# Kernel tuning notes

Hardware: AMD Instinct MI355X
Metric: run time of the kernel (lower is better)

## Reference

```python
import jax, jax.numpy as jnp
import numpy as np

EPS = 1e-8          # EPSILON in source
THRESH = 0.5        # state.match_threshold
MIN_RADIUS = 0.05   # meaningful-observation threshold

B, T, H, D, N = 4, 4096, 2048, 256, 32768
Hq = H // 4


def setup_inputs() -> dict:
    key = jax.random.key(0)
    ks = jax.random.split(key, 10)
    s = 0.02
    return {
        "hidden": jax.random.normal(ks[0], (B, T, H), jnp.float32),
        "beliefs": jax.random.normal(ks[1], (N, D), jnp.float32),
        "active_mask": jax.random.bernoulli(ks[2], 0.5, (N,)),
        "W_obs": jax.random.normal(ks[3], (D, H), jnp.float32) * s,
        "W_g1": jax.random.normal(ks[4], (Hq, H), jnp.float32) * s,
        "b_g1": jnp.zeros((Hq,), jnp.float32),
        "W_g2": jax.random.normal(ks[5], (1, Hq), jnp.float32) * s,
        "b_g2": jnp.full((1,), -2.0, jnp.float32),  # nn.init.constant_(bias, -2.0)
        "W_p1": jax.random.normal(ks[6], (Hq, H), jnp.float32) * s,
        "b_p1": jnp.zeros((Hq,), jnp.float32),
        "W_p2": jax.random.normal(ks[7], (1, Hq), jnp.float32) * s,
        "b_p2": jnp.zeros((1,), jnp.float32),
    }


def reference(hidden, beliefs, active_mask, W_obs, W_g1, b_g1, W_g2, b_g2,
              W_p1, b_p1, W_p2, b_p2):
    # --- projections (torch Linear: y = x @ W.T + b) ---
    obs = jnp.einsum("bth,dh->btd", hidden, W_obs)                       # [B,T,D]
    gate = jax.nn.sigmoid(
        jnp.einsum("btq,oq->bto",
                   jax.nn.relu(jnp.einsum("bth,qh->btq", hidden, W_g1) + b_g1),
                   W_g2) + b_g2)                                          # [B,T,1]
    prec = jax.nn.softplus(
        jnp.einsum("btq,oq->bto",
                   jax.nn.relu(jnp.einsum("bth,qh->btq", hidden, W_p1) + b_p1),
                   W_p2) + b_p2)                                          # [B,T,1]
    gated_prec = gate * prec

    obs_mean = obs.mean(axis=0)          # [T,D]
    prec_mean = gated_prec.mean(axis=0)  # [T,1]
    # F.normalize: x / max(||x||, eps)
    obs_angles = obs_mean / jnp.maximum(
        jnp.linalg.norm(obs_mean, axis=-1, keepdims=True), EPS)
    obs_beliefs = obs_angles * prec_mean  # [T,D] radius = precision

    # --- cosine-similarity 1-NN match against active beliefs ---
    b_radii = jnp.clip(jnp.linalg.norm(beliefs, axis=-1), EPS, None)     # [N]
    b_angles = beliefs / b_radii[:, None]
    o_radii_c = jnp.clip(jnp.linalg.norm(obs_beliefs, axis=-1), EPS, None)
    o_angles = obs_beliefs / o_radii_c[:, None]
    sims = jnp.einsum("td,nd->tn", o_angles, b_angles)                    # [T,N]
    sims_masked = jnp.where(active_mask[None, :], sims, -jnp.inf)
    any_active = jnp.any(active_mask)
    best_sims = jnp.where(any_active, jnp.max(sims_masked, axis=-1), 0.0)  # [T]
    best_global = jnp.where(any_active, jnp.argmax(sims_masked, axis=-1), -1)

    obs_radii = jnp.linalg.norm(obs_beliefs, axis=-1)  # unclamped
    meaningful = obs_radii > MIN_RADIUS
    matched = meaningful & (best_sims > THRESH) & any_active
    slots = jnp.where(matched, best_global, -1)          # matched slot or -1 (new)
    sims_out = jnp.where(matched, best_sims, 0.0)
    return obs_beliefs, sims_out, slots, meaningful
```

## Files before the change

### kernel.cpp

```cpp
#include <hip/hip_runtime.h>
#include <hip/hip_bf16.h>
#include <math.h>

#define TB 4
#define TT 4096
#define HH 2048
#define DD 256
#define NN 32768
#define HQ 512
#define MM (TB*TT)

typedef __attribute__((ext_vector_type(8))) short bf16x8;
typedef __attribute__((ext_vector_type(8))) _Float16 f16x8;
typedef __attribute__((ext_vector_type(4))) float f32x4;

__device__ inline unsigned short f2bf(float x){
  __hip_bfloat16 h = __float2bfloat16(x);
  return *reinterpret_cast<unsigned short*>(&h);
}

__device__ inline unsigned short f2h(float x){
  _Float16 h = (_Float16)x;
  unsigned short u; __builtin_memcpy(&u, &h, 2); return u;
}

__device__ inline bf16x8 as_bf16x8(uint4 u){ bf16x8 r; __builtin_memcpy(&r,&u,16); return r; }

__device__ __forceinline__ void gload_ldsv(const void* g, void* l){
  __builtin_amdgcn_global_load_lds(
      (const __attribute__((address_space(1))) unsigned int*)g,
      (__attribute__((address_space(3))) unsigned int*)l, 16, 0, 0);
}

__global__ __launch_bounds__(256) void k_mean(const float* __restrict__ h,
    unsigned short* __restrict__ hmb){
  const size_t i = (size_t)blockIdx.x*256 + threadIdx.x;
  const size_t TH4 = (size_t)TT*HH/4;
  const float4* p = (const float4*)h;
  float4 v0 = p[i], v1 = p[i+TH4], v2 = p[i+2*TH4], v3 = p[i+3*TH4];
  float4 m;
  m.x = 0.25f*(v0.x+v1.x+v2.x+v3.x);
  m.y = 0.25f*(v0.y+v1.y+v2.y+v3.y);
  m.z = 0.25f*(v0.z+v1.z+v2.z+v3.z);
  m.w = 0.25f*(v0.w+v1.w+v2.w+v3.w);
  ushort4 o; o.x = f2bf(m.x); o.y = f2bf(m.y); o.z = f2bf(m.z); o.w = f2bf(m.w);
  *(ushort4*)(hmb + i*4) = o;
}

#define PREP_CVTW 1024
#define PREP_WOBS 512
#define PREP_BEL  8192
#define PREP_ANY  128
__global__ __launch_bounds__(256) void k_prep(
    const float* __restrict__ Wg1, const float* __restrict__ Wp1,
    unsigned short* __restrict__ Wsw,
    const float* __restrict__ Wobs, unsigned short* __restrict__ wob,
    const float* __restrict__ bel, unsigned short* __restrict__ bbf,
    const unsigned char* __restrict__ mask, int* __restrict__ flag){
  const int b = blockIdx.x;
  if (b < PREP_CVTW){
    const int id = b*256 + threadIdx.x;
    const int n = id >> 8;
    const int cg = id & 255;
    const int k = cg*8;
    const int kc = cg >> 2;
    const int c8 = cg & 3;
    const float* src = (n < HQ) ? (Wg1 + (size_t)n*HH + k) : (Wp1 + (size_t)(n-HQ)*HH + k);
    float4 v0 = *(const float4*)src;
    float4 v1 = *(const float4*)(src + 4);
    unsigned short o[8] = {f2h(v0.x),f2h(v0.y),f2h(v0.z),f2h(v0.w),
                           f2h(v1.x),f2h(v1.y),f2h(v1.z),f2h(v1.w)};
    const int nb = n >> 8, r = n & 255;
    const int s = (r & 3) ^ ((r >> 2) & 3);
    unsigned short* dst = Wsw + ((size_t)(nb*64 + kc))*8192 + r*32 + ((c8 ^ s) << 3);
    __builtin_memcpy(dst, o, 16);
  } else if (b < PREP_CVTW + PREP_WOBS){
    const int idx4 = (b - PREP_CVTW)*256 + threadIdx.x;
    float4 v = *(const float4*)(Wobs + (size_t)idx4*4);
    ushort4 o; o.x = f2bf(v.x); o.y = f2bf(v.y); o.z = f2bf(v.z); o.w = f2bf(v.w);
    *(ushort4*)(wob + (size_t)idx4*4) = o;
  } else if (b < PREP_CVTW + PREP_WOBS + PREP_BEL){
    const int bb = b - (PREP_CVTW + PREP_WOBS);
    const int n = (bb*256 + threadIdx.x) >> 6;
    const int lane = threadIdx.x & 63;
    const float4 v = *(const float4*)(bel + (size_t)n*DD + lane*4);
    float s = v.x*v.x + v.y*v.y + v.z*v.z + v.w*v.w;
    #pragma unroll
    for (int m = 1; m < 64; m <<= 1) s += __shfl_xor(s, m);
    const float inv = 1.f / fmaxf(sqrtf(s), 1e-8f);
    ushort4 o;
    o.x = f2bf(v.x*inv); o.y = f2bf(v.y*inv); o.z = f2bf(v.z*inv); o.w = f2bf(v.w*inv);
    *(ushort4*)(bbf + (size_t)n*DD + lane*4) = o;
  } else {
    const int i = (b - (PREP_CVTW + PREP_WOBS + PREP_BEL))*256 + threadIdx.x;
    const int any = (mask[i] != 0) ? 1 : 0;
    if (__ballot(any)){
      if ((threadIdx.x & 63) == 0) atomicOr(flag, 1);
    }
  }
}

__global__ __launch_bounds__(256) void k_obs(const unsigned short* __restrict__ A,
    const unsigned short* __restrict__ Bw, float* __restrict__ C){
  const int n0 = blockIdx.x*128, m0 = blockIdx.y*128;
  const int tid = threadIdx.x;
  const int w = tid>>6, lane = tid&63, lr = lane&15, q = lane>>4;
  __shared__ __align__(16) unsigned short As[2][4096];
  __shared__ __align__(16) unsigned short Bs[2][4096];
  f32x4 acc[2][8] = {};
  const int srow = lane >> 2;
  const int sch  = (lane & 3) ^ (srow & 3);
  const unsigned short* asrc = A  + (size_t)(m0 + w*32 + srow)*HH + sch*8;
  const unsigned short* bsrc = Bw + (size_t)(n0 + w*32 + srow)*HH + sch*8;

  #pragma unroll
  for (int i = 0; i < 2; i++){
    gload_ldsv(asrc + (size_t)i*16*HH, &As[0][(w*32 + i*16)*32]);
    gload_ldsv(bsrc + (size_t)i*16*HH, &Bs[0][(w*32 + i*16)*32]);
  }
  __syncthreads();

  for (int t = 0; t < 64; t++){
    const int cur = t & 1;
    if (t < 63){
      const int ko = (t+1)*32;
      #pragma unroll
      for (int i = 0; i < 2; i++){
        gload_ldsv(asrc + (size_t)i*16*HH + ko, &As[cur^1][(w*32 + i*16)*32]);
        gload_ldsv(bsrc + (size_t)i*16*HH + ko, &Bs[cur^1][(w*32 + i*16)*32]);
      }
    }
    bf16x8 a[2];
    #pragma unroll
    for (int i = 0; i < 2; i++)
      a[i] = as_bf16x8(*(const uint4*)&As[cur][(w*32 + i*16 + lr)*32 + ((q ^ (lr&3))<<3)]);
    #pragma unroll
    for (int j = 0; j < 8; j++){
      bf16x8 bb = as_bf16x8(*(const uint4*)&Bs[cur][(j*16 + lr)*32 + ((q ^ (lr&3))<<3)]);
      #pragma unroll
      for (int i = 0; i < 2; i++)
        acc[i][j] = __builtin_amdgcn_mfma_f32_16x16x32_bf16(a[i], bb, acc[i][j], 0, 0, 0);
    }
    __syncthreads();
  }
  #pragma unroll
  for (int i = 0; i < 2; i++)
    #pragma unroll
    for (int j = 0; j < 8; j++)
      #pragma unroll
      for (int r = 0; r < 4; r++)
        C[(size_t)(m0 + w*32 + i*16 + q*4 + r)*DD + n0 + j*16 + lr] = acc[i][j][r];
}

__global__ __launch_bounds__(256, 2) void k_gp(const float* __restrict__ A,
    const unsigned short* __restrict__ Wsw,
    const float* __restrict__ bg1, const float* __restrict__ bp1,
    const float* __restrict__ Wg2, const float* __restrict__ Wp2,
    float* __restrict__ z1, float* __restrict__ z2){
  const int bid = blockIdx.x;
  const int nb = (bid >> 3) & 3;
  const int my = (bid & 7) + ((bid >> 5) << 3);
  const int m0 = my*128;
  const int tid = threadIdx.x;
  const int w = tid>>6, lane = tid&63, lr = lane&15, q = lane>>4;
  __shared__ __align__(16) unsigned short Ws[2][8192];
  __shared__ __align__(16) float As[2][4096];
  f32x4 acc[2][16] = {};

  const unsigned short* wt = Wsw + (size_t)nb*64*8192 + w*2048 + lane*8;
  const int rpB = lr*32 + ((q ^ ((lr & 3) ^ ((lr >> 2) & 3))) << 3);
  const int sr8 = lane >> 3;
  const int sc  = (lane & 7) ^ sr8;
  const float* asrc = A + (size_t)(m0 + w*32 + sr8)*HH + sc*4;

  #pragma unroll
  for (int i = 0; i < 4; i++){
    gload_ldsv(wt + i*512, &Ws[0][w*2048 + i*512]);
    gload_ldsv(asrc + (size_t)i*8*HH, &As[0][(w*32 + i*8)*32]);
  }
  __syncthreads();

  for (int t = 0; t < 64; t++){
    const int cur = t & 1;
    if (t < 63){
      #pragma unroll
      for (int i = 0; i < 4; i++){
        gload_ldsv(wt + (size_t)(t+1)*8192 + i*512, &Ws[cur^1][w*2048 + i*512]);
        gload_ldsv(asrc + (size_t)i*8*HH + (t+1)*32, &As[cur^1][(w*32 + i*8)*32]);
      }
    }
    const float* At = As[cur];
    f16x8 ah[2], al[2];
    #pragma unroll
    for (int i = 0; i < 2; i++){
      const int tr = w*32 + i*16 + lr;
      const int px = lr & 7;
      float4 fa = *(const float4*)&At[tr*32 + (((2*q)   ^ px) << 2)];
      float4 fb = *(const float4*)&At[tr*32 + (((2*q+1) ^ px) << 2)];
      float av[8] = {fa.x,fa.y,fa.z,fa.w, fb.x,fb.y,fb.z,fb.w};
      #pragma unroll
      for (int e = 0; e < 8; e++){
        _Float16 h = (_Float16)av[e];
        ah[i][e] = h; al[i][e] = (_Float16)(av[e] - (float)h);
      }
    }
    const unsigned short* Wc = Ws[cur];
    __builtin_amdgcn_s_setprio(1);
    #pragma unroll
    for (int j = 0; j < 16; j++){
      f16x8 bh;
      __builtin_memcpy(&bh, Wc + j*512 + rpB, 16);
      acc[0][j] = __builtin_amdgcn_mfma_f32_16x16x32_f16(ah[0], bh, acc[0][j], 0, 0, 0);
      acc[1][j] = __builtin_amdgcn_mfma_f32_16x16x32_f16(ah[1], bh, acc[1][j], 0, 0, 0);
      acc[0][j] = __builtin_amdgcn_mfma_f32_16x16x32_f16(al[0], bh, acc[0][j], 0, 0, 0);
      acc[1][j] = __builtin_amdgcn_mfma_f32_16x16x32_f16(al[1], bh, acc[1][j], 0, 0, 0);
    }
    __builtin_amdgcn_s_setprio(0);
    __syncthreads();
  }

  const bool isP = (nb >= 2);
  const float* b1 = isP ? bp1 : bg1;
  const float* w2 = isP ? Wp2 : Wg2;
  float* zt = isP ? z2 : z1;
  const int nbl = nb*256 - (isP ? HQ : 0);
  float s[2][4] = {};
  #pragma unroll
  for (int j = 0; j < 16; j++){
    const int n = nbl + j*16 + lr;
    const float bb = b1[n], ww = w2[n];
    #pragma unroll
    for (int i = 0; i < 2; i++)
      #pragma unroll
      for (int r = 0; r < 4; r++)
        s[i][r] += fmaxf(acc[i][j][r] + bb, 0.f) * ww;
  }
  #pragma unroll
  for (int mk = 1; mk < 16; mk <<= 1)
    #pragma unroll
    for (int i = 0; i < 2; i++)
      #pragma unroll
      for (int r = 0; r < 4; r++)
        s[i][r] += __shfl_xor(s[i][r], mk);
  if (lr == 0){
    #pragma unroll
    for (int i = 0; i < 2; i++)
      #pragma unroll
      for (int r = 0; r < 4; r++)
        atomicAdd(&zt[m0 + w*32 + i*16 + q*4 + r], s[i][r]);
  }
}

__global__ __launch_bounds__(256) void k_obs_fin(const float* __restrict__ obs_mean,
    const float* __restrict__ z1, const float* __restrict__ z2,
    const float* __restrict__ bg2, const float* __restrict__ bp2,
    float* __restrict__ out0, float* __restrict__ out3,
    float* __restrict__ obs_radii, unsigned short* __restrict__ obf){
  const int w = threadIdx.x >> 6, lane = threadIdx.x & 63;
  const int t = blockIdx.x*4 + w;
  float pm = 0.f;
  if (lane < TB){
    float a = z1[lane*TT + t] + bg2[0];
    float b = z2[lane*TT + t] + bp2[0];
    float gate = 1.f/(1.f + expf(-a));
    float sp = (b > 0.f) ? (b + log1pf(expf(-b))) : log1pf(expf(b));
    pm = gate * sp;
  }
  #pragma unroll
  for (int m = 1; m < 4; m <<= 1) pm += __shfl_xor(pm, m);
  pm = __shfl(pm, 0) * 0.25f;
  float4 x = *(const float4*)(obs_mean + (size_t)t*DD + lane*4);
  float ss = x.x*x.x + x.y*x.y + x.z*x.z + x.w*x.w;
  #pragma unroll
  for (int m = 1; m < 64; m <<= 1) ss += __shfl_xor(ss, m);
  const float nrm = sqrtf(ss);
  const float sc = pm / fmaxf(nrm, 1e-8f);
  float4 ob = {x.x*sc, x.y*sc, x.z*sc, x.w*sc};
  *(float4*)(out0 + (size_t)t*DD + lane*4) = ob;
  float s2 = ob.x*ob.x + ob.y*ob.y + ob.z*ob.z + ob.w*ob.w;
  #pragma unroll
  for (int m = 1; m < 64; m <<= 1) s2 += __shfl_xor(s2, m);
  const float r2 = sqrtf(s2);
  if (lane == 0){
    obs_radii[t] = r2;
    out3[t] = (r2 > 0.05f) ? 1.f : 0.f;
  }
  const float inv2 = 1.f / fmaxf(r2, 1e-8f);
  ushort4 o = {f2bf(ob.x*inv2), f2bf(ob.y*inv2), f2bf(ob.z*inv2), f2bf(ob.w*inv2)};
  *(ushort4*)(obf + (size_t)t*DD + lane*4) = o;
}

__global__ __launch_bounds__(256) void k_sims(const unsigned short* __restrict__ obf,
    const unsigned short* __restrict__ bbf, const unsigned char* __restrict__ mask,
    float* __restrict__ pmax, int* __restrict__ pidx){
  const int bid = blockIdx.x;
  const int rest = bid >> 3;
  const int ns = (bid & 7) + ((rest >> 5) << 3);
  const int t0 = (rest & 31) * 128;
  const int nbase0 = ns * (NN/32);
  const int tid = threadIdx.x;
  const int w = tid >> 6, lane = tid & 63;
  const int lr = lane & 15, q = lane >> 4;
  __shared__ __align__(16) unsigned short bt[2][32*256];
  __shared__ __align__(16) unsigned char am[1024];
  const int srow = lane >> 5;
  const int sp   = lane & 31;

  ((unsigned int*)am)[tid] = ((const unsigned int*)(mask + nbase0))[tid];

  #pragma unroll
  for (int i = 0; i < 4; i++){
    const int row = (i*4 + w)*2 + srow;
    const unsigned short* src = bbf + (size_t)(nbase0 + row)*DD + ((sp ^ (row & 31)) << 3);
    gload_ldsv(src, &bt[0][(i*4 + w)*512]);
  }
  bf16x8 afr[2][8];
  #pragma unroll
  for (int i = 0; i < 2; i++){
    const unsigned short* ap = obf + (size_t)(t0 + w*32 + i*16 + lr)*DD + q*8;
    #pragma unroll
    for (int ks = 0; ks < 8; ks++)
      afr[i][ks] = as_bf16x8(*(const uint4*)(ap + ks*32));
  }
  __syncthreads();

  float vmax[2][4] = {{-INFINITY,-INFINITY,-INFINITY,-INFINITY},
                      {-INFINITY,-INFINITY,-INFINITY,-INFINITY}};
  int   vidx[2][4] = {{-1,-1,-1,-1},{-1,-1,-1,-1}};
  int cur = 0;
  for (int it = 0; it < 32; it++){
    const int nl = it*32;
    if (it < 31){
      #pragma unroll
      for (int i = 0; i < 4; i++){
        const int row = (i*4 + w)*2 + srow;
        const unsigned short* src = bbf + (size_t)(nbase0 + nl + 32 + row)*DD + ((sp ^ (row & 31)) << 3);
        gload_ldsv(src, &bt[cur^1][(i*4 + w)*512]);
      }
    }
    const unsigned short* btc = bt[cur];
    #pragma unroll
    for (int sub = 0; sub < 2; sub++){
      const int rowi = sub*16 + lr;
      const bool act = (am[nl + rowi] != 0);
      const unsigned short* bp = btc + rowi*256;
      f32x4 acc[2] = {{0.f,0.f,0.f,0.f},{0.f,0.f,0.f,0.f}};
      __builtin_amdgcn_s_setprio(1);
      #pragma unroll
      for (int ks = 0; ks < 8; ks++){
        const int p = (q + ks*4) ^ rowi;
        bf16x8 bfr = as_bf16x8(*(const uint4*)(bp + (p & 31)*8));
        acc[0] = __builtin_amdgcn_mfma_f32_16x16x32_bf16(afr[0][ks], bfr, acc[0], 0, 0, 0);
        acc[1] = __builtin_amdgcn_mfma_f32_16x16x32_bf16(afr[1][ks], bfr, acc[1], 0, 0, 0);
      }
      __builtin_amdgcn_s_setprio(0);
      if (act){
        const int n = nbase0 + nl + rowi;
        #pragma unroll
        for (int i = 0; i < 2; i++)
          #pragma unroll
          for (int r = 0; r < 4; r++)
            if (acc[i][r] > vmax[i][r]){ vmax[i][r] = acc[i][r]; vidx[i][r] = n; }
      }
    }
    __syncthreads();
    cur ^= 1;
  }
  #pragma unroll
  for (int mk = 1; mk < 16; mk <<= 1){
    #pragma unroll
    for (int i = 0; i < 2; i++)
      #pragma unroll
      for (int r = 0; r < 4; r++){
        float om = __shfl_xor(vmax[i][r], mk);
        int   oi = __shfl_xor(vidx[i][r], mk);
        if (om > vmax[i][r] || (om == vmax[i][r] && (unsigned)oi < (unsigned)vidx[i][r])){
          vmax[i][r] = om; vidx[i][r] = oi;
        }
      }
  }
  if (lr == 0){
    #pragma unroll
    for (int i = 0; i < 2; i++)
      #pragma unroll
      for (int r = 0; r < 4; r++){
        const int t = t0 + w*32 + i*16 + q*4 + r;
        pmax[ns*TT + t] = vmax[i][r];
        pidx[ns*TT + t] = vidx[i][r];
      }
  }
}

__global__ __launch_bounds__(256) void k_combine(const float* __restrict__ pmax,
    const int* __restrict__ pidx, const float* __restrict__ obs_radii,
    const int* __restrict__ flag, float* __restrict__ out1, float* __restrict__ out2){
  const int t = blockIdx.x*256 + threadIdx.x;
  float best = -INFINITY; int bi = -1;
  #pragma unroll
  for (int s = 0; s < 32; s++){
    float m = pmax[s*TT + t];
    if (m > best){ best = m; bi = pidx[s*TT + t]; }
  }
  const bool anyA = (flag[0] != 0);
  const bool mf = obs_radii[t] > 0.05f;
  const bool matched = mf && anyA && (best > 0.5f);
  out1[t] = matched ? best : 0.f;
  out2[t] = matched ? (float)bi : -1.f;
}

extern "C" void kernel_launch(void* const* d_in, const int* in_sizes, int n_in,
                              void* d_out, int out_size, void* d_ws, size_t ws_size,
                              hipStream_t stream) {
  const float* hidden = (const float*)d_in[0];
  const float* beliefs = (const float*)d_in[1];
  const unsigned char* amask = (const unsigned char*)d_in[2];
  const float* W_obs = (const float*)d_in[3];
  const float* W_g1 = (const float*)d_in[4];
  const float* b_g1 = (const float*)d_in[5];
  const float* W_g2 = (const float*)d_in[6];
  const float* b_g2 = (const float*)d_in[7];
  const float* W_p1 = (const float*)d_in[8];
  const float* b_p1 = (const float*)d_in[9];
  const float* W_p2 = (const float*)d_in[10];
  const float* b_p2 = (const float*)d_in[11];

  char* ws = (char*)d_ws;
  const size_t HMB_OFF  = 0;
  const size_t WSW_OFF  = 16777216;
  const size_t WOB_OFF  = 20971520;
  const size_t OM_OFF   = 22020096;
  const size_t Z1_OFF   = 26214400;
  const size_t Z2_OFF   = 26279936;
  const size_t FLAG_OFF = 26345472;
  const size_t RAD_OFF  = 26345728;
  const size_t OBF_OFF  = 26362112;
  const size_t BBF_OFF  = 28459264;
  const size_t PMAX_OFF = 45236480;
  const size_t PIDX_OFF = 45760768;

  unsigned short* hmb = (unsigned short*)(ws + HMB_OFF);
  unsigned short* Wsw = (unsigned short*)(ws + WSW_OFF);
  unsigned short* wob = (unsigned short*)(ws + WOB_OFF);
  float* om  = (float*)(ws + OM_OFF);
  float* z1  = (float*)(ws + Z1_OFF);
  float* z2  = (float*)(ws + Z2_OFF);
  int*   flg = (int*)(ws + FLAG_OFF);
  float* rad = (float*)(ws + RAD_OFF);
  unsigned short* obf = (unsigned short*)(ws + OBF_OFF);
  unsigned short* bbf = (unsigned short*)(ws + BBF_OFF);
  float* pmax = (float*)(ws + PMAX_OFF);
  int*   pidx = (int*)(ws + PIDX_OFF);

  float* out0 = (float*)d_out;
  float* out1 = out0 + (size_t)TT*DD;
  float* out2 = out1 + TT;
  float* out3 = out2 + TT;

  hipMemsetAsync(ws + Z1_OFF, 0, 2*MM*sizeof(float) + 256, stream);

  k_prep    <<<PREP_CVTW + PREP_WOBS + PREP_BEL + PREP_ANY, 256, 0, stream>>>(
                W_g1, W_p1, Wsw, W_obs, wob, beliefs, bbf, amask, flg);
  k_mean    <<<TT*HH/4/256, 256, 0, stream>>>(hidden, hmb);
  k_obs     <<<dim3(DD/128, TT/128), 256, 0, stream>>>(hmb, wob, om);
  k_gp      <<<512, 256, 0, stream>>>(hidden, Wsw, b_g1, b_p1, W_g2, W_p2, z1, z2);
  k_obs_fin <<<TT/4, 256, 0, stream>>>(om, z1, z2, b_g2, b_p2, out0, out3, rad, obf);
  k_sims    <<<1024, 256, 0, stream>>>(obf, bbf, amask, pmax, pidx);
  k_combine <<<TT/256, 256, 0, stream>>>(pmax, pidx, rad, flg, out1, out2);
}
```

Before: 502.1 us.

## Fuse mean, zeroing and obs finalize into fewer launches; retile obs GEMM

Folds the batch-mean kernel and the memset of the gate/precision accumulators and flag into the prep kernel. The obs GEMM becomes full-row 64x256 tiles so its epilogue can compute the row norm, gate/precision combination and bf16 angle output directly, which removes the separate finalize kernel and the fp32 obs intermediate. The active-mask flag is moved into extra blocks of the obs kernel, and k_gp reorders its loads and pairs B fragments in its MFMA loop. The aim is fewer launches and less global traffic, at the cost of only 64 GEMM blocks for the obs projection, which may underfill the GPU.

```diff
diff --git a/kernel.cpp b/kernel.cpp
--- a/kernel.cpp
+++ b/kernel.cpp
@@ -32,34 +32,34 @@
       (__attribute__((address_space(3))) unsigned int*)l, 16, 0, 0);
 }
 
-__global__ __launch_bounds__(256) void k_mean(const float* __restrict__ h,
-    unsigned short* __restrict__ hmb){
-  const size_t i = (size_t)blockIdx.x*256 + threadIdx.x;
-  const size_t TH4 = (size_t)TT*HH/4;
-  const float4* p = (const float4*)h;
-  float4 v0 = p[i], v1 = p[i+TH4], v2 = p[i+2*TH4], v3 = p[i+3*TH4];
-  float4 m;
-  m.x = 0.25f*(v0.x+v1.x+v2.x+v3.x);
-  m.y = 0.25f*(v0.y+v1.y+v2.y+v3.y);
-  m.z = 0.25f*(v0.z+v1.z+v2.z+v3.z);
-  m.w = 0.25f*(v0.w+v1.w+v2.w+v3.w);
-  ushort4 o; o.x = f2bf(m.x); o.y = f2bf(m.y); o.z = f2bf(m.z); o.w = f2bf(m.w);
-  *(ushort4*)(hmb + i*4) = o;
-}
-
+#define PREP_MEAN 8192
 #define PREP_CVTW 1024
 #define PREP_WOBS 512
 #define PREP_BEL  8192
-#define PREP_ANY  128
+#define PREP_ZERO 129
+#define PREP_GRID (PREP_MEAN+PREP_CVTW+PREP_WOBS+PREP_BEL+PREP_ZERO)
 __global__ __launch_bounds__(256) void k_prep(
+    const float* __restrict__ h, unsigned short* __restrict__ hmb,
     const float* __restrict__ Wg1, const float* __restrict__ Wp1,
     unsigned short* __restrict__ Wsw,
     const float* __restrict__ Wobs, unsigned short* __restrict__ wob,
     const float* __restrict__ bel, unsigned short* __restrict__ bbf,
-    const unsigned char* __restrict__ mask, int* __restrict__ flag){
+    unsigned int* __restrict__ zbase){
   const int b = blockIdx.x;
-  if (b < PREP_CVTW){
-    const int id = b*256 + threadIdx.x;
+  if (b < PREP_MEAN){
+    const size_t i = (size_t)b*256 + threadIdx.x;
+    const size_t TH4 = (size_t)TT*HH/4;
+    const float4* p = (const float4*)h;
+    float4 v0 = p[i], v1 = p[i+TH4], v2 = p[i+2*TH4], v3 = p[i+3*TH4];
+    float4 m;
+    m.x = 0.25f*(v0.x+v1.x+v2.x+v3.x);
+    m.y = 0.25f*(v0.y+v1.y+v2.y+v3.y);
+    m.z = 0.25f*(v0.z+v1.z+v2.z+v3.z);
+    m.w = 0.25f*(v0.w+v1.w+v2.w+v3.w);
+    ushort4 o; o.x = f2bf(m.x); o.y = f2bf(m.y); o.z = f2bf(m.z); o.w = f2bf(m.w);
+    *(ushort4*)(hmb + i*4) = o;
+  } else if (b < PREP_MEAN + PREP_CVTW){
+    const int id = (b - PREP_MEAN)*256 + threadIdx.x;
     const int n = id >> 8;
     const int cg = id & 255;
     const int k = cg*8;
@@ -74,13 +74,13 @@
     const int s = (r & 3) ^ ((r >> 2) & 3);
     unsigned short* dst = Wsw + ((size_t)(nb*64 + kc))*8192 + r*32 + ((c8 ^ s) << 3);
     __builtin_memcpy(dst, o, 16);
-  } else if (b < PREP_CVTW + PREP_WOBS){
-    const int idx4 = (b - PREP_CVTW)*256 + threadIdx.x;
+  } else if (b < PREP_MEAN + PREP_CVTW + PREP_WOBS){
+    const int idx4 = (b - PREP_MEAN - PREP_CVTW)*256 + threadIdx.x;
     float4 v = *(const float4*)(Wobs + (size_t)idx4*4);
     ushort4 o; o.x = f2bf(v.x); o.y = f2bf(v.y); o.z = f2bf(v.z); o.w = f2bf(v.w);
     *(ushort4*)(wob + (size_t)idx4*4) = o;
-  } else if (b < PREP_CVTW + PREP_WOBS + PREP_BEL){
-    const int bb = b - (PREP_CVTW + PREP_WOBS);
+  } else if (b < PREP_MEAN + PREP_CVTW + PREP_WOBS + PREP_BEL){
+    const int bb = b - (PREP_MEAN + PREP_CVTW + PREP_WOBS);
     const int n = (bb*256 + threadIdx.x) >> 6;
     const int lane = threadIdx.x & 63;
     const float4 v = *(const float4*)(bel + (size_t)n*DD + lane*4);
@@ -92,64 +92,101 @@
     o.x = f2bf(v.x*inv); o.y = f2bf(v.y*inv); o.z = f2bf(v.z*inv); o.w = f2bf(v.w*inv);
     *(ushort4*)(bbf + (size_t)n*DD + lane*4) = o;
   } else {
-    const int i = (b - (PREP_CVTW + PREP_WOBS + PREP_BEL))*256 + threadIdx.x;
+    const int idx = (b - (PREP_MEAN + PREP_CVTW + PREP_WOBS + PREP_BEL))*256 + threadIdx.x;
+    if (idx < 32832) zbase[idx] = 0;
+  }
+}
+
+__global__ __launch_bounds__(256) void k_obs(const unsigned short* __restrict__ A,
+    const unsigned short* __restrict__ Bw,
+    const float* __restrict__ z1, const float* __restrict__ z2,
+    const float* __restrict__ bg2, const float* __restrict__ bp2,
+    float* __restrict__ out0, float* __restrict__ out3,
+    unsigned short* __restrict__ obf,
+    const unsigned char* __restrict__ mask, int* __restrict__ flag){
+  const int blk = blockIdx.x;
+  const int tid = threadIdx.x;
+  if (blk >= 64){
+    const int i = (blk - 64)*256 + tid;
     const int any = (mask[i] != 0) ? 1 : 0;
     if (__ballot(any)){
-      if ((threadIdx.x & 63) == 0) atomicOr(flag, 1);
-    }
-  }
-}
-
-__global__ __launch_bounds__(256) void k_obs(const unsigned short* __restrict__ A,
-    const unsigned short* __restrict__ Bw, float* __restrict__ C){
-  const int n0 = blockIdx.x*128, m0 = blockIdx.y*128;
-  const int tid = threadIdx.x;
+      if ((tid & 63) == 0) atomicOr(flag, 1);
+    }
+    return;
+  }
+  const int m0 = blk*64;
   const int w = tid>>6, lane = tid&63, lr = lane&15, q = lane>>4;
-  __shared__ __align__(16) unsigned short As[2][4096];
-  __shared__ __align__(16) unsigned short Bs[2][4096];
-  f32x4 acc[2][8] = {};
-  const int srow = lane >> 2;
-  const int sch  = (lane & 3) ^ (srow & 3);
-  const unsigned short* asrc = A  + (size_t)(m0 + w*32 + srow)*HH + sch*8;
-  const unsigned short* bsrc = Bw + (size_t)(n0 + w*32 + srow)*HH + sch*8;
-
-  #pragma unroll
-  for (int i = 0; i < 2; i++){
-    gload_ldsv(asrc + (size_t)i*16*HH, &As[0][(w*32 + i*16)*32]);
-    gload_ldsv(bsrc + (size_t)i*16*HH, &Bs[0][(w*32 + i*16)*32]);
+  __shared__ __align__(16) unsigned short As[2][64*32];
+  __shared__ __align__(16) unsigned short Bs[2][256*32];
+  f32x4 acc[16] = {};
+  const int srow = lane >> 2, sch = (lane & 3) ^ (srow & 3);
+  const unsigned short* asrc = A + (size_t)(m0 + w*16 + srow)*HH + sch*8;
+
+  gload_ldsv(asrc, &As[0][w*16*32]);
+  #pragma unroll
+  for (int i = 0; i < 4; i++){
+    const unsigned short* bsrc = Bw + (size_t)((i*4 + w)*16 + srow)*HH + sch*8;
+    gload_ldsv(bsrc, &Bs[0][(i*4 + w)*16*32]);
   }
   __syncthreads();
-
+  const int px = (q ^ (lr & 3)) << 3;
   for (int t = 0; t < 64; t++){
     const int cur = t & 1;
     if (t < 63){
       const int ko = (t+1)*32;
-      #pragma unroll
-      for (int i = 0; i < 2; i++){
-        gload_ldsv(asrc + (size_t)i*16*HH + ko, &As[cur^1][(w*32 + i*16)*32]);
-        gload_ldsv(bsrc + (size_t)i*16*HH + ko, &Bs[cur^1][(w*32 + i*16)*32]);
-      }
-    }
-    bf16x8 a[2];
-    #pragma unroll
-    for (int i = 0; i < 2; i++)
-      a[i] = as_bf16x8(*(const uint4*)&As[cur][(w*32 + i*16 + lr)*32 + ((q ^ (lr&3))<<3)]);
-    #pragma unroll
-    for (int j = 0; j < 8; j++){
-      bf16x8 bb = as_bf16x8(*(const uint4*)&Bs[cur][(j*16 + lr)*32 + ((q ^ (lr&3))<<3)]);
-      #pragma unroll
-      for (int i = 0; i < 2; i++)
-        acc[i][j] = __builtin_amdgcn_mfma_f32_16x16x32_bf16(a[i], bb, acc[i][j], 0, 0, 0);
+      gload_ldsv(asrc + ko, &As[cur^1][w*16*32]);
+      #pragma unroll
+      for (int i = 0; i < 4; i++){
+        const unsigned short* bsrc = Bw + (size_t)((i*4 + w)*16 + srow)*HH + ko + sch*8;
+        gload_ldsv(bsrc, &Bs[cur^1][(i*4 + w)*16*32]);
+      }
+    }
+    bf16x8 a = as_bf16x8(*(const uint4*)&As[cur][(w*16 + lr)*32 + px]);
+    #pragma unroll
+    for (int j = 0; j < 16; j++){
+      bf16x8 bb = as_bf16x8(*(const uint4*)&Bs[cur][(j*16 + lr)*32 + px]);
+      acc[j] = __builtin_amdgcn_mfma_f32_16x16x32_bf16(a, bb, acc[j], 0, 0, 0);
     }
     __syncthreads();
   }
   #pragma unroll
-  for (int i = 0; i < 2; i++)
-    #pragma unroll
-    for (int j = 0; j < 8; j++)
-      #pragma unroll
-      for (int r = 0; r < 4; r++)
-        C[(size_t)(m0 + w*32 + i*16 + q*4 + r)*DD + n0 + j*16 + lr] = acc[i][j][r];
+  for (int r = 0; r < 4; r++){
+    const int t = m0 + w*16 + q*4 + r;
+    float s2 = 0.f;
+    #pragma unroll
+    for (int j = 0; j < 16; j++) s2 += acc[j][r]*acc[j][r];
+    #pragma unroll
+    for (int mk = 1; mk < 16; mk <<= 1) s2 += __shfl_xor(s2, mk);
+    const float nrm = sqrtf(s2);
+    float p = 0.f;
+    #pragma unroll
+    for (int bb = 0; bb < TB; bb++){
+      float a = z1[bb*TT + t] + bg2[0];
+      float c = z2[bb*TT + t] + bp2[0];
+      float gate = 1.f/(1.f + expf(-a));
+      float sp = (c > 0.f) ? (c + log1pf(expf(-c))) : log1pf(expf(c));
+      p += gate * sp;
+    }
+    const float pm = p * 0.25f;
+    const float sc = pm / fmaxf(nrm, 1e-8f);
+    float qq = 0.f;
+    #pragma unroll
+    for (int j = 0; j < 16; j++){
+      float o = acc[j][r] * sc;
+      out0[(size_t)t*DD + j*16 + lr] = o;
+      qq += o*o;
+    }
+    #pragma unroll
+    for (int mk = 1; mk < 16; mk <<= 1) qq += __shfl_xor(qq, mk);
+    const float r2 = sqrtf(qq);
+    const float inv2 = 1.f / fmaxf(r2, 1e-8f);
+    #pragma unroll
+    for (int j = 0; j < 16; j++){
+      float o = acc[j][r] * sc;
+      obf[(size_t)t*DD + j*16 + lr] = f2bf(o * inv2);
+    }
+    if (lr == 0) out3[t] = (r2 > 0.05f) ? 1.f : 0.f;
+  }
 }
 
 __global__ __launch_bounds__(256, 2) void k_gp(const float* __restrict__ A,
@@ -174,29 +211,29 @@
   const float* asrc = A + (size_t)(m0 + w*32 + sr8)*HH + sc*4;
 
   #pragma unroll
-  for (int i = 0; i < 4; i++){
-    gload_ldsv(wt + i*512, &Ws[0][w*2048 + i*512]);
-    gload_ldsv(asrc + (size_t)i*8*HH, &As[0][(w*32 + i*8)*32]);
-  }
+  for (int i = 0; i < 4; i++) gload_ldsv(asrc + (size_t)i*8*HH, &As[0][(w*32 + i*8)*32]);
+  #pragma unroll
+  for (int i = 0; i < 4; i++) gload_ldsv(wt + i*512, &Ws[0][w*2048 + i*512]);
   __syncthreads();
 
   for (int t = 0; t < 64; t++){
     const int cur = t & 1;
     if (t < 63){
       #pragma unroll
-      for (int i = 0; i < 4; i++){
+      for (int i = 0; i < 4; i++)
+        gload_ldsv(asrc + (size_t)i*8*HH + (t+1)*32, &As[cur^1][(w*32 + i*8)*32]);
+      #pragma unroll
+      for (int i = 0; i < 4; i++)
         gload_ldsv(wt + (size_t)(t+1)*8192 + i*512, &Ws[cur^1][w*2048 + i*512]);
-        gload_ldsv(asrc + (size_t)i*8*HH + (t+1)*32, &As[cur^1][(w*32 + i*8)*32]);
-      }
     }
     const float* At = As[cur];
     f16x8 ah[2], al[2];
     #pragma unroll
     for (int i = 0; i < 2; i++){
       const int tr = w*32 + i*16 + lr;
-      const int px = lr & 7;
-      float4 fa = *(const float4*)&At[tr*32 + (((2*q)   ^ px) << 2)];
-      float4 fb = *(const float4*)&At[tr*32 + (((2*q+1) ^ px) << 2)];
+      const int pxx = lr & 7;
+      float4 fa = *(const float4*)&At[tr*32 + (((2*q)   ^ pxx) << 2)];
+      float4 fb = *(const float4*)&At[tr*32 + (((2*q+1) ^ pxx) << 2)];
       float av[8] = {fa.x,fa.y,fa.z,fa.w, fb.x,fb.y,fb.z,fb.w};
       #pragma unroll
       for (int e = 0; e < 8; e++){
@@ -207,20 +244,25 @@
     const unsigned short* Wc = Ws[cur];
     __builtin_amdgcn_s_setprio(1);
     #pragma unroll
-    for (int j = 0; j < 16; j++){
-      f16x8 bh;
-      __builtin_memcpy(&bh, Wc + j*512 + rpB, 16);
-      acc[0][j] = __builtin_amdgcn_mfma_f32_16x16x32_f16(ah[0], bh, acc[0][j], 0, 0, 0);
-      acc[1][j] = __builtin_amdgcn_mfma_f32_16x16x32_f16(ah[1], bh, acc[1][j], 0, 0, 0);
-      acc[0][j] = __builtin_amdgcn_mfma_f32_16x16x32_f16(al[0], bh, acc[0][j], 0, 0, 0);
-      acc[1][j] = __builtin_amdgcn_mfma_f32_16x16x32_f16(al[1], bh, acc[1][j], 0, 0, 0);
+    for (int jp = 0; jp < 8; jp++){
+      f16x8 b0, b1;
+      __builtin_memcpy(&b0, Wc + (2*jp)*512 + rpB, 16);
+      __builtin_memcpy(&b1, Wc + (2*jp+1)*512 + rpB, 16);
+      acc[0][2*jp]   = __builtin_amdgcn_mfma_f32_16x16x32_f16(ah[0], b0, acc[0][2*jp],   0, 0, 0);
+      acc[1][2*jp]   = __builtin_amdgcn_mfma_f32_16x16x32_f16(ah[1], b0, acc[1][2*jp],   0, 0, 0);
+      acc[0][2*jp+1] = __builtin_amdgcn_mfma_f32_16x16x32_f16(ah[0], b1, acc[0][2*jp+1], 0, 0, 0);
+      acc[1][2*jp+1] = __builtin_amdgcn_mfma_f32_16x16x32_f16(ah[1], b1, acc[1][2*jp+1], 0, 0, 0);
+      acc[0][2*jp]   = __builtin_amdgcn_mfma_f32_16x16x32_f16(al[0], b0, acc[0][2*jp],   0, 0, 0);
+      acc[1][2*jp]   = __builtin_amdgcn_mfma_f32_16x16x32_f16(al[1], b0, acc[1][2*jp],   0, 0, 0);
+      acc[0][2*jp+1] = __builtin_amdgcn_mfma_f32_16x16x32_f16(al[0], b1, acc[0][2*jp+1], 0, 0, 0);
+      acc[1][2*jp+1] = __builtin_amdgcn_mfma_f32_16x16x32_f16(al[1], b1, acc[1][2*jp+1], 0, 0, 0);
     }
     __builtin_amdgcn_s_setprio(0);
     __syncthreads();
   }
 
   const bool isP = (nb >= 2);
-  const float* b1 = isP ? bp1 : bg1;
+  const float* b1p = isP ? bp1 : bg1;
   const float* w2 = isP ? Wp2 : Wg2;
   float* zt = isP ? z2 : z1;
   const int nbl = nb*256 - (isP ? HQ : 0);
@@ -228,7 +270,7 @@
   #pragma unroll
   for (int j = 0; j < 16; j++){
     const int n = nbl + j*16 + lr;
-    const float bb = b1[n], ww = w2[n];
+    const float bb = b1p[n], ww = w2[n];
     #pragma unroll
     for (int i = 0; i < 2; i++)
       #pragma unroll
@@ -249,45 +291,6 @@
       for (int r = 0; r < 4; r++)
         atomicAdd(&zt[m0 + w*32 + i*16 + q*4 + r], s[i][r]);
   }
-}
-
-__global__ __launch_bounds__(256) void k_obs_fin(const float* __restrict__ obs_mean,
-    const float* __restrict__ z1, const float* __restrict__ z2,
-    const float* __restrict__ bg2, const float* __restrict__ bp2,
-    float* __restrict__ out0, float* __restrict__ out3,
-    float* __restrict__ obs_radii, unsigned short* __restrict__ obf){
-  const int w = threadIdx.x >> 6, lane = threadIdx.x & 63;
-  const int t = blockIdx.x*4 + w;
-  float pm = 0.f;
-  if (lane < TB){
-    float a = z1[lane*TT + t] + bg2[0];
-    float b = z2[lane*TT + t] + bp2[0];
-    float gate = 1.f/(1.f + expf(-a));
-    float sp = (b > 0.f) ? (b + log1pf(expf(-b))) : log1pf(expf(b));
-    pm = gate * sp;
-  }
-  #pragma unroll
-  for (int m = 1; m < 4; m <<= 1) pm += __shfl_xor(pm, m);
-  pm = __shfl(pm, 0) * 0.25f;
-  float4 x = *(const float4*)(obs_mean + (size_t)t*DD + lane*4);
-  float ss = x.x*x.x + x.y*x.y + x.z*x.z + x.w*x.w;
-  #pragma unroll
-  for (int m = 1; m < 64; m <<= 1) ss += __shfl_xor(ss, m);
-  const float nrm = sqrtf(ss);
-  const float sc = pm / fmaxf(nrm, 1e-8f);
-  float4 ob = {x.x*sc, x.y*sc, x.z*sc, x.w*sc};
-  *(float4*)(out0 + (size_t)t*DD + lane*4) = ob;
-  float s2 = ob.x*ob.x + ob.y*ob.y + ob.z*ob.z + ob.w*ob.w;
-  #pragma unroll
-  for (int m = 1; m < 64; m <<= 1) s2 += __shfl_xor(s2, m);
-  const float r2 = sqrtf(s2);
-  if (lane == 0){
-    obs_radii[t] = r2;
-    out3[t] = (r2 > 0.05f) ? 1.f : 0.f;
-  }
-  const float inv2 = 1.f / fmaxf(r2, 1e-8f);
-  ushort4 o = {f2bf(ob.x*inv2), f2bf(ob.y*inv2), f2bf(ob.z*inv2), f2bf(ob.w*inv2)};
-  *(ushort4*)(obf + (size_t)t*DD + lane*4) = o;
 }
 
 __global__ __launch_bounds__(256) void k_sims(const unsigned short* __restrict__ obf,
@@ -392,7 +395,7 @@
 }
 
 __global__ __launch_bounds__(256) void k_combine(const float* __restrict__ pmax,
-    const int* __restrict__ pidx, const float* __restrict__ obs_radii,
+    const int* __restrict__ pidx, const float* __restrict__ out3,
     const int* __restrict__ flag, float* __restrict__ out1, float* __restrict__ out2){
   const int t = blockIdx.x*256 + threadIdx.x;
   float best = -INFINITY; int bi = -1;
@@ -402,7 +405,7 @@
     if (m > best){ best = m; bi = pidx[s*TT + t]; }
   }
   const bool anyA = (flag[0] != 0);
-  const bool mf = obs_radii[t] > 0.05f;
+  const bool mf = out3[t] != 0.f;
   const bool matched = mf && anyA && (best > 0.5f);
   out1[t] = matched ? best : 0.f;
   out2[t] = matched ? (float)bi : -1.f;
@@ -428,11 +431,9 @@
   const size_t HMB_OFF  = 0;
   const size_t WSW_OFF  = 16777216;
   const size_t WOB_OFF  = 20971520;
-  const size_t OM_OFF   = 22020096;
   const size_t Z1_OFF   = 26214400;
   const size_t Z2_OFF   = 26279936;
   const size_t FLAG_OFF = 26345472;
-  const size_t RAD_OFF  = 26345728;
   const size_t OBF_OFF  = 26362112;
   const size_t BBF_OFF  = 28459264;
   const size_t PMAX_OFF = 45236480;
@@ -441,11 +442,9 @@
   unsigned short* hmb = (unsigned short*)(ws + HMB_OFF);
   unsigned short* Wsw = (unsigned short*)(ws + WSW_OFF);
   unsigned short* wob = (unsigned short*)(ws + WOB_OFF);
-  float* om  = (float*)(ws + OM_OFF);
   float* z1  = (float*)(ws + Z1_OFF);
   float* z2  = (float*)(ws + Z2_OFF);
   int*   flg = (int*)(ws + FLAG_OFF);
-  float* rad = (float*)(ws + RAD_OFF);
   unsigned short* obf = (unsigned short*)(ws + OBF_OFF);
   unsigned short* bbf = (unsigned short*)(ws + BBF_OFF);
   float* pmax = (float*)(ws + PMAX_OFF);
@@ -456,14 +455,11 @@
   float* out2 = out1 + TT;
   float* out3 = out2 + TT;
 
-  hipMemsetAsync(ws + Z1_OFF, 0, 2*MM*sizeof(float) + 256, stream);
-
-  k_prep    <<<PREP_CVTW + PREP_WOBS + PREP_BEL + PREP_ANY, 256, 0, stream>>>(
-                W_g1, W_p1, Wsw, W_obs, wob, beliefs, bbf, amask, flg);
-  k_mean    <<<TT*HH/4/256, 256, 0, stream>>>(hidden, hmb);
-  k_obs     <<<dim3(DD/128, TT/128), 256, 0, stream>>>(hmb, wob, om);
+  k_prep    <<<PREP_GRID, 256, 0, stream>>>(hidden, hmb, W_g1, W_p1, Wsw,
+                W_obs, wob, beliefs, bbf, (unsigned int*)z1);
   k_gp      <<<512, 256, 0, stream>>>(hidden, Wsw, b_g1, b_p1, W_g2, W_p2, z1, z2);
-  k_obs_fin <<<TT/4, 256, 0, stream>>>(om, z1, z2, b_g2, b_p2, out0, out3, rad, obf);
+  k_obs     <<<64 + NN/256, 256, 0, stream>>>(hmb, wob, z1, z2, b_g2, b_p2,
+                out0, out3, obf, amask, flg);
   k_sims    <<<1024, 256, 0, stream>>>(obf, bbf, amask, pmax, pidx);
-  k_combine <<<TT/256, 256, 0, stream>>>(pmax, pidx, rad, flg, out1, out2);
-}
+  k_combine <<<TT/256, 256, 0, stream>>>(pmax, pidx, out3, flg, out1, out2);
+}
```

Measured after the change: 511.4 us. Within noise of the previous version (+1.8%).
